# Optimization experiments

Hardware: AMD Instinct MI355X
Metric: run time of the kernel (lower is better)

The kernel has to match this reference:

```python
import jax, jax.numpy as jnp
import numpy as np

B, S, H, NH = 2, 2048, 1024, 16
DK = H // NH

def setup_inputs() -> dict:
    key = jax.random.key(0)
    ks = jax.random.split(key, 8)
    scale = 0.02
    return {
        "x": jax.random.normal(ks[0], (B, S, H), jnp.float32),
        "mask": jax.random.randint(ks[1], (B, S, S), 0, 2, jnp.int32),
        "alibi": jax.random.normal(ks[2], (1, NH, S, S), jnp.float32),
        "W_q": jax.random.normal(ks[3], (H, H), jnp.float32) * scale,
        "b_q": jnp.zeros((H,), jnp.float32),
        "W_k": jax.random.normal(ks[4], (H, H), jnp.float32) * scale,
        "b_k": jnp.zeros((H,), jnp.float32),
        "W_v": jax.random.normal(ks[5], (H, H), jnp.float32) * scale,
        "b_v": jnp.zeros((H,), jnp.float32),
        "W_o": jax.random.normal(ks[6], (H, H), jnp.float32) * scale,
        "b_o": jnp.zeros((H,), jnp.float32),
    }

def reference(x, mask, alibi, W_q, b_q, W_k, b_k, W_v, b_v, W_o, b_o):
    b, s, h = x.shape
    def split_heads(t):  # [B,S,H] -> [B,NH,S,DK]
        return t.reshape(b, s, NH, DK).transpose(0, 2, 1, 3)
    q = split_heads(x @ W_q + b_q)
    k = split_heads(x @ W_k + b_k)
    v = split_heads(x @ W_v + b_v)
    scores = jnp.einsum("bhqd,bhkd->bhqk", q, k) / jnp.sqrt(jnp.float32(DK))
    scores = scores + alibi
    scores = jnp.where(mask[:, None, :, :] == 0, jnp.float32(-1e9), scores)
    probs = jax.nn.softmax(scores, axis=-1)  # dropout is identity in eval
    ctx = jnp.einsum("bhqk,bhkd->bhqd", probs, v)
    ctx = ctx.transpose(0, 2, 1, 3).reshape(b, s, h)
    return ctx @ W_o + b_o
```

## Files before the change

kernel.cpp:

```cpp
#include <hip/hip_runtime.h>
#include <hip/hip_bf16.h>


#define S_LEN 2048
#define H_DIM 1024
#define N_HEADS 16

typedef __bf16 bf16x8 __attribute__((ext_vector_type(8)));
typedef __bf16 bf16x4 __attribute__((ext_vector_type(4)));
typedef float f32x4 __attribute__((ext_vector_type(4)));
typedef unsigned long long u64;

using gvoid = __attribute__((address_space(1))) void;
using svoid = __attribute__((address_space(3))) void;

static __device__ __forceinline__ f32x4 mfma16(bf16x8 a, bf16x8 b, f32x4 c) {
  return __builtin_amdgcn_mfma_f32_16x16x32_bf16(a, b, c, 0, 0, 0);
}

template <int NCH, int NW>
static __device__ __forceinline__ void stage64(const __bf16* g, int rstride,
                                               __bf16* lds, int wid, int lane) {
#pragma unroll
  for (int i = 0; i < NCH / NW; ++i) {
    int chunk = i * NW + wid;
    int u = chunk * 64 + lane;
    int r = u >> 3, s = u & 7;
    const __bf16* src = g + (size_t)r * rstride + ((s ^ (r & 7)) << 3);
    __builtin_amdgcn_global_load_lds((const gvoid*)src,
                                     (svoid*)(lds + chunk * 512), 16, 0, 0);
  }
}

static __device__ __forceinline__ bf16x8 read_frag(const __bf16* lds, int r,
                                                   int slot) {
  return *(const bf16x8*)(lds + r * 64 + ((slot ^ (r & 7)) << 3));
}

__global__ __launch_bounds__(256) void k_convert_x(const float* __restrict__ x,
                                                   __bf16* __restrict__ xb) {
  size_t idx = ((size_t)blockIdx.x * 256 + threadIdx.x) * 8;
  float4 a = *(const float4*)(x + idx);
  float4 b = *(const float4*)(x + idx + 4);
  bf16x8 o;
  o[0] = (__bf16)a.x; o[1] = (__bf16)a.y; o[2] = (__bf16)a.z; o[3] = (__bf16)a.w;
  o[4] = (__bf16)b.x; o[5] = (__bf16)b.y; o[6] = (__bf16)b.z; o[7] = (__bf16)b.w;
  *(bf16x8*)(xb + idx) = o;
}

__global__ __launch_bounds__(256) void k_transpose_w(
    const float* __restrict__ w0, const float* __restrict__ w1,
    const float* __restrict__ w2, const float* __restrict__ w3,
    __bf16* __restrict__ wt) {
  __shared__ float t[64][65];
  int z = blockIdx.z;
  const float* W = (z == 0) ? w0 : (z == 1) ? w1 : (z == 2) ? w2 : w3;
  __bf16* O = wt + (size_t)z * H_DIM * H_DIM;
  int k0 = blockIdx.x * 64, n0 = blockIdx.y * 64;
  int tid = threadIdx.x;
  {
    int r = tid >> 4, c4 = tid & 15;
#pragma unroll
    for (int i = 0; i < 4; ++i) {
      float4 v = *(const float4*)(W + (size_t)(k0 + r + i * 16) * H_DIM + n0 + c4 * 4);
      t[r + i * 16][c4 * 4 + 0] = v.x;
      t[r + i * 16][c4 * 4 + 1] = v.y;
      t[r + i * 16][c4 * 4 + 2] = v.z;
      t[r + i * 16][c4 * 4 + 3] = v.w;
    }
  }
  __syncthreads();
  {
    int nn = tid >> 2, js = (tid & 3) * 16;
    bf16x8 o0, o1;
#pragma unroll
    for (int j = 0; j < 8; ++j) {
      o0[j] = (__bf16)t[js + j][nn];
      o1[j] = (__bf16)t[js + 8 + j][nn];
    }
    __bf16* dst = O + (size_t)(n0 + nn) * H_DIM + k0 + js;
    *(bf16x8*)dst = o0;
    *(bf16x8*)(dst + 8) = o1;
  }
}

__global__ __launch_bounds__(256) void k_transpose_v(const __bf16* __restrict__ V,
                                                     __bf16* __restrict__ VT) {
  __shared__ __bf16 t[64][65];
  int bh = blockIdx.y;
  int s0 = blockIdx.x * 64;
  const __bf16* Vb = V + (size_t)bh * S_LEN * 64;
  int tid = threadIdx.x;
#pragma unroll
  for (int i = 0; i < 2; ++i) {
    int u = i * 256 + tid;
    int r = u >> 3, c8 = u & 7;
    bf16x8 v = *(const bf16x8*)(Vb + (size_t)(s0 + r) * 64 + c8 * 8);
#pragma unroll
    for (int j = 0; j < 8; ++j) t[r][c8 * 8 + j] = v[j];
  }
  __syncthreads();
  int d = tid >> 2, js = (tid & 3) * 16;
  bf16x8 o0, o1;
#pragma unroll
  for (int j = 0; j < 8; ++j) {
    o0[j] = t[js + j][d];
    o1[j] = t[js + 8 + j][d];
  }
  __bf16* dst = VT + (size_t)bh * 64 * S_LEN + (size_t)d * S_LEN + s0 + js;
  *(bf16x8*)dst = o0;
  *(bf16x8*)(dst + 8) = o1;
}

__global__ __launch_bounds__(256) void k_pack_mask(const int* __restrict__ m,
                                                   u64* __restrict__ out) {
  size_t idx = (size_t)blockIdx.x * 256 + threadIdx.x;
  u64 b = __ballot(m[idx] != 0);
  if ((threadIdx.x & 63) == 0) out[idx >> 6] = b;
}

template <int MODE>
__global__ __launch_bounds__(256) void k_gemm(
    const __bf16* __restrict__ A, const __bf16* __restrict__ B0,
    const __bf16* __restrict__ B1, const __bf16* __restrict__ B2,
    const float* __restrict__ bias0, const float* __restrict__ bias1,
    const float* __restrict__ bias2, __bf16* __restrict__ O0,
    __bf16* __restrict__ O1, __bf16* __restrict__ O2, float* __restrict__ Of) {
  __shared__ alignas(16) __bf16 As[128 * 64];
  __shared__ alignas(16) __bf16 Bs[128 * 64];
  int tid = threadIdx.x, wid = tid >> 6, lane = tid & 63;
  int l15 = lane & 15, lg = lane >> 4;
  int nbase = blockIdx.x * 128, mbase = blockIdx.y * 128;
  const __bf16* Bm;
  const float* bias;
  __bf16* Ob;
  float oscale = 1.0f;
  if (MODE == 0) {
    int z = blockIdx.z;
    Bm = (z == 0) ? B0 : (z == 1) ? B1 : B2;
    bias = (z == 0) ? bias0 : (z == 1) ? bias1 : bias2;
    Ob = (z == 0) ? O0 : (z == 1) ? O1 : O2;
    if (z == 0) oscale = 0.125f;
  } else {
    Bm = B0; bias = bias0; Ob = O0;
  }
  int wrow = wid >> 1, wcol = wid & 1;
  f32x4 zero = {0.f, 0.f, 0.f, 0.f};
  f32x4 acc[4][4];
#pragma unroll
  for (int i = 0; i < 4; ++i)
#pragma unroll
    for (int j = 0; j < 4; ++j) acc[i][j] = zero;

  for (int kb = 0; kb < H_DIM; kb += 64) {
    __syncthreads();
    const __bf16* Abase;
    int arstride;
    if (MODE == 0) {
      Abase = A + (size_t)mbase * H_DIM + kb;
      arstride = H_DIM;
    } else {
      int b = mbase >> 11, q0 = mbase & 2047, head = kb >> 6;
      Abase = A + ((size_t)(b * N_HEADS + head) * S_LEN + q0) * 64;
      arstride = 64;
    }
    stage64<16, 4>(Abase, arstride, As, wid, lane);
    stage64<16, 4>(Bm + (size_t)nbase * H_DIM + kb, H_DIM, Bs, wid, lane);
    __syncthreads();
#pragma unroll
    for (int t = 0; t < 2; ++t) {
      bf16x8 a[4], bfr[4];
#pragma unroll
      for (int i = 0; i < 4; ++i)
        a[i] = read_frag(As, wrow * 64 + i * 16 + l15, t * 4 + lg);
#pragma unroll
      for (int j = 0; j < 4; ++j)
        bfr[j] = read_frag(Bs, wcol * 64 + j * 16 + l15, t * 4 + lg);
#pragma unroll
      for (int i = 0; i < 4; ++i)
#pragma unroll
        for (int j = 0; j < 4; ++j) acc[i][j] = mfma16(a[i], bfr[j], acc[i][j]);
    }
  }
  float bv[4];
#pragma unroll
  for (int j = 0; j < 4; ++j) bv[j] = bias[nbase + wcol * 64 + j * 16 + l15];
#pragma unroll
  for (int i = 0; i < 4; ++i)
#pragma unroll
    for (int j = 0; j < 4; ++j)
#pragma unroll
      for (int r = 0; r < 4; ++r) {
        int m = mbase + wrow * 64 + i * 16 + lg * 4 + r;
        int col = nbase + wcol * 64 + j * 16 + l15;
        float v = (acc[i][j][r] + bv[j]) * oscale;
        if (MODE == 0) {
          size_t off =
              (((size_t)(m >> 11) * N_HEADS + (col >> 6)) * S_LEN + (m & 2047)) * 64 +
              (col & 63);
          Ob[off] = (__bf16)v;
        } else {
          Of[(size_t)m * H_DIM + col] = v;
        }
      }
}

__global__ __launch_bounds__(512) void k_attn(
    const __bf16* __restrict__ Q, const __bf16* __restrict__ K,
    const __bf16* __restrict__ VT, const float* __restrict__ alibi,
    const u64* __restrict__ maskb, float* __restrict__ Op,
    float* __restrict__ ml) {
  __shared__ alignas(16) __bf16 Ks[2][64 * 64];
  __shared__ alignas(16) __bf16 Vs[64 * 64];
  __shared__ alignas(16) __bf16 Ps[8][16 * 64];
  int tid = threadIdx.x, wid = tid >> 6, lane = tid & 63;
  int l15 = lane & 15, lg = lane >> 4;
  int bh = blockIdx.x;
  int b = bh & 1, h = bh >> 1;
  int qbase = blockIdx.y * 128;
  const int z = blockIdx.z;
  size_t bho = (size_t)(b * N_HEADS + h);
  const __bf16* Qb = Q + bho * S_LEN * 64;
  const __bf16* Kbz = K + (bho * S_LEN + (size_t)z * 1024) * 64;
  const __bf16* Vbz = VT + bho * 64 * S_LEN + z * 1024;
  const int q = qbase + wid * 16 + l15;
  const int NT = 16;

  bf16x8 qa[2];
  {
    const __bf16* qrow = Qb + (size_t)q * 64;
    qa[0] = *(const bf16x8*)(qrow + lg * 8);
    qa[1] = *(const bf16x8*)(qrow + 32 + lg * 8);
  }
  float mrun = -__builtin_inff(), lrun = 0.f;
  f32x4 cacc[4];
  f32x4 zero = {0.f, 0.f, 0.f, 0.f};
#pragma unroll
  for (int c = 0; c < 4; ++c) cacc[c] = zero;

  const float* arow =
      alibi + ((size_t)h * S_LEN + q) * S_LEN + z * 1024 + lg * 4;
  const u64* mrow =
      maskb + ((size_t)b * S_LEN + q) * (S_LEN / 64) + z * 16;

  char* pbase = (char*)&Ps[wid][0] + l15 * 128;

  stage64<8, 8>(Kbz, 64, Ks[0], wid, lane);
  __builtin_amdgcn_sched_barrier(0);
  f32x4 albP[4];
  u64 mskP;
#pragma unroll
  for (int c = 0; c < 4; ++c) albP[c] = *(const f32x4*)(arow + c * 16);
  mskP = mrow[0];
  __builtin_amdgcn_sched_barrier(0);

  for (int t = 0; t < NT; ++t) {
    const int cur = t & 1;
    asm volatile("s_waitcnt vmcnt(5)" ::: "memory");
    __builtin_amdgcn_sched_barrier(0);
    __builtin_amdgcn_s_barrier();
    __builtin_amdgcn_sched_barrier(0);
    stage64<8, 8>(Vbz + t * 64, S_LEN, Vs, wid, lane);
    __builtin_amdgcn_sched_barrier(0);
    const int tn = (t + 1 < NT) ? t + 1 : t;
    stage64<8, 8>(Kbz + (size_t)tn * 64 * 64, 64, Ks[cur ^ 1], wid, lane);
    __builtin_amdgcn_sched_barrier(0);

    f32x4 sacc[4];
#pragma unroll
    for (int c = 0; c < 4; ++c) sacc[c] = albP[c];
    __builtin_amdgcn_s_setprio(1);
#pragma unroll
    for (int t2 = 0; t2 < 2; ++t2) {
      bf16x8 kf[4];
#pragma unroll
      for (int c = 0; c < 4; ++c)
        kf[c] = read_frag(Ks[cur], c * 16 + l15, t2 * 4 + lg);
#pragma unroll
      for (int c = 0; c < 4; ++c) sacc[c] = mfma16(kf[c], qa[t2], sacc[c]);
    }
    __builtin_amdgcn_s_setprio(0);
    u64 sh = mskP >> (lg * 4);
#pragma unroll
    for (int c = 0; c < 4; ++c)
      albP[c] = *(const f32x4*)(arow + tn * 64 + c * 16);
    mskP = mrow[tn];

    float s[4][4];
    float m16 = -__builtin_inff();
#pragma unroll
    for (int c = 0; c < 4; ++c) {
      unsigned bits = (unsigned)(sh >> (c * 16)) & 0xFu;
#pragma unroll
      for (int r = 0; r < 4; ++r) {
        float v = (bits & (1u << r)) ? sacc[c][r] : -1e9f;
        s[c][r] = v;
        m16 = fmaxf(m16, v);
      }
    }
    m16 = fmaxf(m16, __shfl_xor(m16, 16));
    m16 = fmaxf(m16, __shfl_xor(m16, 32));
    const bool norsc = __all(m16 <= mrun);
    float mn = fmaxf(mrun, m16);
    float scl = __expf(mrun - mn);
    mrun = mn;
    float rs = 0.f;
#pragma unroll
    for (int c = 0; c < 4; ++c)
#pragma unroll
      for (int r = 0; r < 4; ++r) {
        float pe = __expf(s[c][r] - mn);
        s[c][r] = pe;
        rs += pe;
      }
    rs += __shfl_xor(rs, 16);
    rs += __shfl_xor(rs, 32);
    lrun = lrun * scl + rs;
    if (!norsc) {
#pragma unroll
      for (int c = 0; c < 4; ++c) {
        f32x4 v = cacc[c];
        v[0] *= scl; v[1] *= scl; v[2] *= scl; v[3] *= scl;
        cacc[c] = v;
      }
    }
#pragma unroll
    for (int c = 0; c < 4; ++c) {
      bf16x4 u;
#pragma unroll
      for (int r = 0; r < 4; ++r) u[r] = (__bf16)s[c][r];
      int slot = 2 * c + (lg >> 1);
      *(bf16x4*)(pbase + (((slot ^ (l15 & 7)) << 4) | ((lg & 1) << 3))) = u;
    }
    __builtin_amdgcn_sched_barrier(0);
    asm volatile("s_waitcnt vmcnt(6)" ::: "memory");
    __builtin_amdgcn_sched_barrier(0);
    __builtin_amdgcn_s_barrier();
    __builtin_amdgcn_sched_barrier(0);
    __builtin_amdgcn_s_setprio(1);
#pragma unroll
    for (int t2 = 0; t2 < 2; ++t2) {
      bf16x8 pa =
          *(const bf16x8*)(pbase + (((4 * t2 + lg) ^ (l15 & 7)) << 4));
#pragma unroll
      for (int c = 0; c < 4; ++c) {
        bf16x8 vb = read_frag(Vs, c * 16 + l15, t2 * 4 + lg);
        cacc[c] = mfma16(vb, pa, cacc[c]);
      }
    }
    __builtin_amdgcn_s_setprio(0);
  }
  asm volatile("s_waitcnt vmcnt(0)" ::: "memory");
  float* op = Op + (((size_t)z * 32 + bho) * S_LEN + q) * 64;
#pragma unroll
  for (int c = 0; c < 4; ++c) *(f32x4*)(op + c * 16 + lg * 4) = cacc[c];
  if (lg == 0) {
    float2* mlp = (float2*)(ml + (((size_t)z * 32 + bho) * S_LEN + q) * 2);
    *mlp = make_float2(mrun, lrun);
  }
}

__global__ __launch_bounds__(256) void k_combine(const float* __restrict__ Op,
                                                 const float* __restrict__ ml,
                                                 __bf16* __restrict__ ctx) {
  int t = blockIdx.x * 256 + threadIdx.x;
  int dgrp = t & 15, qq = t >> 4;
  float2 m0 = *(const float2*)(ml + (size_t)qq * 2);
  float2 m1 = *(const float2*)(ml + ((size_t)65536 + qq) * 2);
  float m = fmaxf(m0.x, m1.x);
  float e0 = __expf(m0.x - m), e1 = __expf(m1.x - m);
  float inv = 1.f / (m0.y * e0 + m1.y * e1);
  f32x4 a = *(const f32x4*)(Op + (size_t)qq * 64 + dgrp * 4);
  f32x4 c = *(const f32x4*)(Op + (size_t)65536 * 64 + (size_t)qq * 64 + dgrp * 4);
  bf16x4 o;
#pragma unroll
  for (int j = 0; j < 4; ++j) o[j] = (__bf16)((a[j] * e0 + c[j] * e1) * inv);
  *(bf16x4*)(ctx + (size_t)qq * 64 + dgrp * 4) = o;
}

extern "C" void kernel_launch(void* const* d_in, const int* in_sizes, int n_in,
                              void* d_out, int out_size, void* d_ws,
                              size_t ws_size, hipStream_t stream) {
  const float* x = (const float*)d_in[0];
  const int* mask = (const int*)d_in[1];
  const float* alibi = (const float*)d_in[2];
  const float* Wq = (const float*)d_in[3];
  const float* bq = (const float*)d_in[4];
  const float* Wk = (const float*)d_in[5];
  const float* bk = (const float*)d_in[6];
  const float* Wv = (const float*)d_in[7];
  const float* bv = (const float*)d_in[8];
  const float* Wo = (const float*)d_in[9];
  const float* bo = (const float*)d_in[10];
  float* out = (float*)d_out;
  char* ws = (char*)d_ws;

  const size_t MB = 1u << 20;
  __bf16* xb = (__bf16*)(ws);
  __bf16* wt = (__bf16*)(ws + 8 * MB);
  __bf16* Qb = (__bf16*)(ws + 16 * MB);
  __bf16* Kb = (__bf16*)(ws + 24 * MB);
  __bf16* Vb = (__bf16*)(ws + 32 * MB);
  __bf16* VTb = (__bf16*)(ws + 40 * MB);
  float* Op = (float*)(ws + 48 * MB);
  float* mlb = (float*)(ws + 112 * MB);
  __bf16* ctxb = xb;
  __bf16* wtq = wt;
  __bf16* wtk = wt + (1u << 20);
  __bf16* wtv = wt + 2 * (1u << 20);
  __bf16* wto = wt + 3 * (1u << 20);
  u64* maskb = (u64*)Vb;

  k_convert_x<<<dim3(2048), 256, 0, stream>>>(x, xb);
  k_transpose_w<<<dim3(16, 16, 4), 256, 0, stream>>>(Wq, Wk, Wv, Wo, wt);
  k_gemm<0><<<dim3(8, 32, 3), 256, 0, stream>>>(xb, wtq, wtk, wtv, bq, bk, bv,
                                                Qb, Kb, Vb, nullptr);
  k_transpose_v<<<dim3(32, 32), 256, 0, stream>>>(Vb, VTb);
  k_pack_mask<<<dim3((2 * S_LEN * S_LEN) / 256), 256, 0, stream>>>(mask, maskb);
  k_attn<<<dim3(32, 16, 2), 512, 0, stream>>>(Qb, Kb, VTb, alibi, maskb, Op,
                                              mlb);
  k_combine<<<dim3(4096), 256, 0, stream>>>(Op, mlb, ctxb);
  k_gemm<1><<<dim3(8, 32, 1), 256, 0, stream>>>(ctxb, wto, nullptr, nullptr, bo,
                                                nullptr, nullptr, nullptr,
                                                nullptr, nullptr, out);
}
```

Baseline: 250.4 us.

## Shrink attention tiles to 64 queries and 32 keys with double-buffered V

Reworks the attention kernel to use 256-thread blocks covering 64 queries, iterating over 32-key tiles instead of 64. V is now double-buffered in LDS alongside K and prefetched one tile ahead, which removes the second per-iteration block barrier before the PV MFMA. Each wave reads its own P row back without a block barrier. This doubles the grid and cuts LDS per block, which should raise occupancy and overlap, at the cost of twice as many loop iterations and smaller MFMA batches per barrier.

```diff
diff --git a/kernel.cpp b/kernel.cpp
--- a/kernel.cpp
+++ b/kernel.cpp
@@ -35,6 +35,20 @@
 static __device__ __forceinline__ bf16x8 read_frag(const __bf16* lds, int r,
                                                    int slot) {
   return *(const bf16x8*)(lds + r * 64 + ((slot ^ (r & 7)) << 3));
+}
+
+static __device__ __forceinline__ void stage32v(const __bf16* g, __bf16* lds,
+                                                int chunk, int lane) {
+  int u = chunk * 64 + lane;
+  int r = u >> 2, s = u & 3;
+  const __bf16* src = g + (size_t)r * S_LEN + ((s ^ (r & 3)) << 3);
+  __builtin_amdgcn_global_load_lds((const gvoid*)src,
+                                   (svoid*)(lds + chunk * 512), 16, 0, 0);
+}
+
+static __device__ __forceinline__ bf16x8 read_frag32(const __bf16* lds, int r,
+                                                     int slot) {
+  return *(const bf16x8*)(lds + r * 32 + ((slot ^ (r & 3)) << 3));
 }
 
 __global__ __launch_bounds__(256) void k_convert_x(const float* __restrict__ x,
@@ -205,26 +219,26 @@
       }
 }
 
-__global__ __launch_bounds__(512) void k_attn(
+__global__ __launch_bounds__(256) void k_attn(
     const __bf16* __restrict__ Q, const __bf16* __restrict__ K,
     const __bf16* __restrict__ VT, const float* __restrict__ alibi,
     const u64* __restrict__ maskb, float* __restrict__ Op,
     float* __restrict__ ml) {
-  __shared__ alignas(16) __bf16 Ks[2][64 * 64];
-  __shared__ alignas(16) __bf16 Vs[64 * 64];
-  __shared__ alignas(16) __bf16 Ps[8][16 * 64];
+  __shared__ alignas(16) __bf16 Ks[2][32 * 64];
+  __shared__ alignas(16) __bf16 Vs[2][64 * 32];
+  __shared__ alignas(16) __bf16 Ps[4][16 * 32];
   int tid = threadIdx.x, wid = tid >> 6, lane = tid & 63;
   int l15 = lane & 15, lg = lane >> 4;
   int bh = blockIdx.x;
   int b = bh & 1, h = bh >> 1;
-  int qbase = blockIdx.y * 128;
+  int qbase = blockIdx.y * 64;
   const int z = blockIdx.z;
   size_t bho = (size_t)(b * N_HEADS + h);
   const __bf16* Qb = Q + bho * S_LEN * 64;
   const __bf16* Kbz = K + (bho * S_LEN + (size_t)z * 1024) * 64;
   const __bf16* Vbz = VT + bho * 64 * S_LEN + z * 1024;
   const int q = qbase + wid * 16 + l15;
-  const int NT = 16;
+  const int NT = 32;
 
   bf16x8 qa[2];
   {
@@ -240,61 +254,59 @@
 
   const float* arow =
       alibi + ((size_t)h * S_LEN + q) * S_LEN + z * 1024 + lg * 4;
-  const u64* mrow =
-      maskb + ((size_t)b * S_LEN + q) * (S_LEN / 64) + z * 16;
-
-  char* pbase = (char*)&Ps[wid][0] + l15 * 128;
-
-  stage64<8, 8>(Kbz, 64, Ks[0], wid, lane);
+  const unsigned* mrow =
+      (const unsigned*)(maskb + ((size_t)b * S_LEN + q) * (S_LEN / 64)) + z * 32;
+
+  char* pbase = (char*)&Ps[wid][0] + l15 * 64;
+
+  stage32v(Vbz, Vs[0], wid, lane);
+  stage64<4, 4>(Kbz, 64, Ks[0], wid, lane);
   __builtin_amdgcn_sched_barrier(0);
-  f32x4 albP[4];
-  u64 mskP;
-#pragma unroll
-  for (int c = 0; c < 4; ++c) albP[c] = *(const f32x4*)(arow + c * 16);
+  f32x4 albP[2];
+  unsigned mskP;
+  albP[0] = *(const f32x4*)(arow);
+  albP[1] = *(const f32x4*)(arow + 16);
   mskP = mrow[0];
   __builtin_amdgcn_sched_barrier(0);
 
   for (int t = 0; t < NT; ++t) {
     const int cur = t & 1;
-    asm volatile("s_waitcnt vmcnt(5)" ::: "memory");
+    asm volatile("s_waitcnt vmcnt(3)" ::: "memory");
     __builtin_amdgcn_sched_barrier(0);
     __builtin_amdgcn_s_barrier();
     __builtin_amdgcn_sched_barrier(0);
-    stage64<8, 8>(Vbz + t * 64, S_LEN, Vs, wid, lane);
+    const int kn = ((t + 1 < NT) ? t + 1 : t) * 32;
+    stage32v(Vbz + kn, Vs[cur ^ 1], wid, lane);
+    stage64<4, 4>(Kbz + (size_t)kn * 64, 64, Ks[cur ^ 1], wid, lane);
     __builtin_amdgcn_sched_barrier(0);
-    const int tn = (t + 1 < NT) ? t + 1 : t;
-    stage64<8, 8>(Kbz + (size_t)tn * 64 * 64, 64, Ks[cur ^ 1], wid, lane);
-    __builtin_amdgcn_sched_barrier(0);
-
-    f32x4 sacc[4];
-#pragma unroll
-    for (int c = 0; c < 4; ++c) sacc[c] = albP[c];
+
+    f32x4 sacc[2];
+#pragma unroll
+    for (int c = 0; c < 2; ++c) sacc[c] = albP[c];
     __builtin_amdgcn_s_setprio(1);
 #pragma unroll
     for (int t2 = 0; t2 < 2; ++t2) {
-      bf16x8 kf[4];
-#pragma unroll
-      for (int c = 0; c < 4; ++c)
+      bf16x8 kf[2];
+#pragma unroll
+      for (int c = 0; c < 2; ++c)
         kf[c] = read_frag(Ks[cur], c * 16 + l15, t2 * 4 + lg);
 #pragma unroll
-      for (int c = 0; c < 4; ++c) sacc[c] = mfma16(kf[c], qa[t2], sacc[c]);
+      for (int c = 0; c < 2; ++c) sacc[c] = mfma16(kf[c], qa[t2], sacc[c]);
     }
     __builtin_amdgcn_s_setprio(0);
-    u64 sh = mskP >> (lg * 4);
-#pragma unroll
-    for (int c = 0; c < 4; ++c)
-      albP[c] = *(const f32x4*)(arow + tn * 64 + c * 16);
-    mskP = mrow[tn];
-
-    float s[4][4];
+    unsigned shm = mskP >> (lg * 4);
+    albP[0] = *(const f32x4*)(arow + kn);
+    albP[1] = *(const f32x4*)(arow + kn + 16);
+    mskP = mrow[(t + 1 < NT) ? t + 1 : t];
+
     float m16 = -__builtin_inff();
 #pragma unroll
-    for (int c = 0; c < 4; ++c) {
-      unsigned bits = (unsigned)(sh >> (c * 16)) & 0xFu;
+    for (int c = 0; c < 2; ++c) {
+      unsigned bits = (shm >> (c * 16)) & 0xFu;
 #pragma unroll
       for (int r = 0; r < 4; ++r) {
         float v = (bits & (1u << r)) ? sacc[c][r] : -1e9f;
-        s[c][r] = v;
+        sacc[c][r] = v;
         m16 = fmaxf(m16, v);
       }
     }
@@ -306,11 +318,11 @@
     mrun = mn;
     float rs = 0.f;
 #pragma unroll
-    for (int c = 0; c < 4; ++c)
+    for (int c = 0; c < 2; ++c)
 #pragma unroll
       for (int r = 0; r < 4; ++r) {
-        float pe = __expf(s[c][r] - mn);
-        s[c][r] = pe;
+        float pe = __expf(sacc[c][r] - mn);
+        sacc[c][r] = pe;
         rs += pe;
       }
     rs += __shfl_xor(rs, 16);
@@ -325,28 +337,19 @@
       }
     }
 #pragma unroll
+    for (int c = 0; c < 2; ++c) {
+      bf16x4 u;
+#pragma unroll
+      for (int r = 0; r < 4; ++r) u[r] = (__bf16)sacc[c][r];
+      int slot = 2 * c + (lg >> 1);
+      *(bf16x4*)(pbase + (((slot ^ (l15 & 3)) << 4) | ((lg & 1) << 3))) = u;
+    }
+    bf16x8 pa = *(const bf16x8*)(pbase + (((lg ^ (l15 & 3))) << 4));
+    __builtin_amdgcn_s_setprio(1);
+#pragma unroll
     for (int c = 0; c < 4; ++c) {
-      bf16x4 u;
-#pragma unroll
-      for (int r = 0; r < 4; ++r) u[r] = (__bf16)s[c][r];
-      int slot = 2 * c + (lg >> 1);
-      *(bf16x4*)(pbase + (((slot ^ (l15 & 7)) << 4) | ((lg & 1) << 3))) = u;
-    }
-    __builtin_amdgcn_sched_barrier(0);
-    asm volatile("s_waitcnt vmcnt(6)" ::: "memory");
-    __builtin_amdgcn_sched_barrier(0);
-    __builtin_amdgcn_s_barrier();
-    __builtin_amdgcn_sched_barrier(0);
-    __builtin_amdgcn_s_setprio(1);
-#pragma unroll
-    for (int t2 = 0; t2 < 2; ++t2) {
-      bf16x8 pa =
-          *(const bf16x8*)(pbase + (((4 * t2 + lg) ^ (l15 & 7)) << 4));
-#pragma unroll
-      for (int c = 0; c < 4; ++c) {
-        bf16x8 vb = read_frag(Vs, c * 16 + l15, t2 * 4 + lg);
-        cacc[c] = mfma16(vb, pa, cacc[c]);
-      }
+      bf16x8 vb = read_frag32(Vs[cur], c * 16 + l15, lg);
+      cacc[c] = mfma16(vb, pa, cacc[c]);
     }
     __builtin_amdgcn_s_setprio(0);
   }
@@ -417,7 +420,7 @@
                                                 Qb, Kb, Vb, nullptr);
   k_transpose_v<<<dim3(32, 32), 256, 0, stream>>>(Vb, VTb);
   k_pack_mask<<<dim3((2 * S_LEN * S_LEN) / 256), 256, 0, stream>>>(mask, maskb);
-  k_attn<<<dim3(32, 16, 2), 512, 0, stream>>>(Qb, Kb, VTb, alibi, maskb, Op,
+  k_attn<<<dim3(32, 32, 2), 256, 0, stream>>>(Qb, Kb, VTb, alibi, maskb, Op,
                                               mlb);
   k_combine<<<dim3(4096), 256, 0, stream>>>(Op, mlb, ctxb);
   k_gemm<1><<<dim3(8, 32, 1), 256, 0, stream>>>(ctxb, wto, nullptr, nullptr, bo,
```

After: 279.0 us. 1.11x slower.
